# Kernel optimization log

Measured on AMD Instinct MI355X. Metric: run time of the kernel, lower is better.

The kernel has to match this reference:

```python
import jax, jax.numpy as jnp
import numpy as np

B, IN, HID, OUT, K = 4096, 1024, 2048, 256, 8
# pairwise (i, j), i != j, row-major order as in the torch loop
_PAIRS = np.array([(i, j) for i in range(K) for j in range(K) if i != j])  # [56, 2]
IDX_I = jnp.asarray(_PAIRS[:, 0])
IDX_J = jnp.asarray(_PAIRS[:, 1])


def setup_inputs() -> dict:
    key = jax.random.key(0)
    ks = jax.random.split(key, 13)
    s_in, s_hid, s_2o, s_o = IN ** -0.5, HID ** -0.5, (2 * OUT) ** -0.5, OUT ** -0.5
    return {
        "input": jax.random.normal(ks[0], (B, IN), jnp.float32),
        # 8 stacked branch MLPs
        "W1": jax.random.normal(ks[1], (K, IN, HID), jnp.float32) * s_in,
        "b1": jax.random.normal(ks[2], (K, HID), jnp.float32) * s_in,
        "W2": jax.random.normal(ks[3], (K, HID, OUT), jnp.float32) * s_hid,
        "b2": jax.random.normal(ks[4], (K, OUT), jnp.float32) * s_hid,
        # model_on: 2*OUT -> HID -> 1
        "Won1": jax.random.normal(ks[5], (2 * OUT, HID), jnp.float32) * s_2o,
        "bon1": jax.random.normal(ks[6], (HID,), jnp.float32) * s_2o,
        "Won2": jax.random.normal(ks[7], (HID, 1), jnp.float32) * s_hid,
        "bon2": jax.random.normal(ks[8], (1,), jnp.float32) * s_hid,
        # model_clear: OUT -> HID -> 1
        "Wc1": jax.random.normal(ks[9], (OUT, HID), jnp.float32) * s_o,
        "bc1": jax.random.normal(ks[10], (HID,), jnp.float32) * s_o,
        "Wc2": jax.random.normal(ks[11], (HID, 1), jnp.float32) * s_hid,
        "bc2": jax.random.normal(ks[12], (1,), jnp.float32) * s_hid,
    }


def reference(input, W1, b1, W2, b2, Won1, bon1, Won2, bon2, Wc1, bc1, Wc2, bc2):
    # 8 branch MLPs on the same input, as one grouped GEMM: [K, B, HID]
    h = jax.nn.relu(jnp.einsum('bi,kih->kbh', input, W1) + b1[:, None, :])
    emb = jnp.einsum('kbh,kho->kbo', h, W2) + b2[:, None, :]  # [K, B, OUT]

    # 56 pairwise concats -> model_on, batched: [56, B, 2*OUT]
    pair = jnp.concatenate([emb[IDX_I], emb[IDX_J]], axis=-1)
    ho = jax.nn.relu(jnp.einsum('pbf,fh->pbh', pair, Won1) + bon1)
    on = jnp.einsum('pbh,h->pb', ho, Won2[:, 0]) + bon2[0]  # [56, B]

    # 8 clear heads, batched: [8, B]
    hc = jax.nn.relu(jnp.einsum('kbo,oh->kbh', emb, Wc1) + bc1)
    clear = jnp.einsum('kbh,h->kb', hc, Wc2[:, 0]) + bc2[0]

    # torch concatenates [56 on-outputs, 8 clear-outputs] along dim=1 -> [B, 64]
    return jnp.concatenate([on, clear], axis=0).T
```

## Files before the change

kernel.cpp:

```cpp
#include <hip/hip_runtime.h>

typedef __attribute__((ext_vector_type(8))) short bf16x8;
typedef __attribute__((ext_vector_type(4))) float f32x4;
typedef __attribute__((ext_vector_type(8))) unsigned short u16x8;

__device__ __forceinline__ float bf2f(short s) {
  unsigned u = ((unsigned)(unsigned short)s) << 16;
  return __builtin_bit_cast(float, u);
}
__device__ __forceinline__ unsigned short f2bf(float f) {
  unsigned u = __builtin_bit_cast(unsigned, f);
  u = (u + 0x7fffu + ((u >> 16) & 1u)) >> 16;
  return (unsigned short)u;
}
__device__ __forceinline__ void gload16(const unsigned short* g, unsigned short* l) {
  __builtin_amdgcn_global_load_lds(
      (const __attribute__((address_space(1))) void*)g,
      (__attribute__((address_space(3))) void*)l, 16, 0, 0);
}

__global__ __launch_bounds__(256)
void prep_kernel(const float* __restrict__ input, const float* __restrict__ W1,
                 const float* __restrict__ W2, const float* __restrict__ Won1,
                 const float* __restrict__ Wc1,
                 unsigned short* __restrict__ inputb, unsigned short* __restrict__ W1T,
                 unsigned short* __restrict__ W2T, unsigned short* __restrict__ WcatT,
                 unsigned short* __restrict__ Wc1T) {
  int bid = blockIdx.x;
  const int t = threadIdx.x;
  if (bid < 2048) {
    long i = ((long)bid * 256 + t) * 8;
    float4 a = *(const float4*)(input + i);
    float4 b = *(const float4*)(input + i + 4);
    u16x8 o;
    o[0] = f2bf(a.x); o[1] = f2bf(a.y); o[2] = f2bf(a.z); o[3] = f2bf(a.w);
    o[4] = f2bf(b.x); o[5] = f2bf(b.y); o[6] = f2bf(b.z); o[7] = f2bf(b.w);
    *(u16x8*)(inputb + i) = o;
    return;
  }
  bid -= 2048;
  const float* src; unsigned short* dst;
  int R, C, tilesX, tilesY; long sb, db;
  if (bid < 16384) {
    src = W1; dst = W1T; R = 1024; C = 2048; tilesX = 64; tilesY = 32;
    sb = 2097152; db = 2097152;
  } else if ((bid -= 16384) < 4096) {
    src = W2; dst = W2T; R = 2048; C = 256; tilesX = 8; tilesY = 64;
    sb = 524288; db = 524288;
  } else if ((bid -= 4096) < 512) {
    src = Won1; dst = WcatT; R = 256; C = 2048; tilesX = 64; tilesY = 8;
    sb = 0; db = 0;
  } else if ((bid -= 512) < 512) {
    src = Won1 + 524288; dst = WcatT + (long)2048 * 256;
    R = 256; C = 2048; tilesX = 64; tilesY = 8; sb = 0; db = 0;
  } else {
    bid -= 512;
    src = Wc1; dst = Wc1T; R = 256; C = 2048; tilesX = 64; tilesY = 8;
    sb = 0; db = 0;
  }
  const int x = bid % tilesX;
  const int rem = bid / tilesX;
  const int y = rem % tilesY;
  const int z = rem / tilesY;
  src += (long)z * sb;
  dst += (long)z * db;
  __shared__ float tile[32][33];
  const int tx = t & 31, ty = t >> 5;
  const int bx = x * 32, by = y * 32;
  #pragma unroll
  for (int i = ty; i < 32; i += 8)
    tile[i][tx] = src[(long)(by + i) * C + bx + tx];
  __syncthreads();
  #pragma unroll
  for (int i = ty; i < 32; i += 8)
    dst[(long)(bx + i) * R + by + tx] = f2bf(tile[tx][i]);
}

template<bool HAS_BIAS, bool RELU>
__global__ __launch_bounds__(512, 1)
void gemm256(const unsigned short* __restrict__ A,
             const unsigned short* __restrict__ Bt,
             const float* __restrict__ bias,
             unsigned short* __restrict__ C,
             int N, int K, int nx, int ny, int GM,
             long sA, long sB, long sBias, long sC) {
  __shared__ unsigned short lds[65536];
  const int t = threadIdx.x;
  const int lane = t & 63;
  const int w = t >> 6, wr = w >> 2, wc = w & 3;

  const int nwg = gridDim.x;
  const int cpx = nwg >> 3;
  const int id = blockIdx.x;
  const int sw = (id & 7) * cpx + (id >> 3);
  const int z = sw / (nx * ny);
  const int rem = sw % (nx * ny);
  const int band = rem / (GM * nx);
  const int rr = rem % (GM * nx);
  const int y = band * GM + (rr % GM);
  const int x = rr / GM;
  const int m0 = y * 256, n0 = x * 256;

  A += (long)z * sA;
  Bt += (long)z * sB;
  C += (long)z * sC;

  const int NH = K >> 4;
  const int ITERS = K >> 7;

  const int sr0 = t >> 3;
  const int sc0 = (t & 7) * 16;
  const int cks0 = (((lane >> 4) * 16)) ^ ((lane & 7) << 4);
  const int cks1 = (64 + ((lane >> 4) * 16)) ^ ((lane & 7) << 4);
  const int aoff = wr * 16384 + (lane & 15) * 128;
  const int boff = 32768 + (wc >> 1) * 16384 + ((wc & 1) * 64 + (lane & 15)) * 128;

  f32x4 acc[8][4] = {};
  bf16x8 af[4][2];
  bf16x8 bfr[2][2][2];

#define STAGE(S) do { if ((S) < NH) {                                          \
    const int kt_ = (S) >> 2, slot_ = (S) & 3;                                 \
    const int base_ = ((kt_ & 1) << 16) + ((slot_ < 2) ? 32768 : 0)            \
                      + ((slot_ & 1) << 14);                                   \
    const unsigned short* gb_;                                                 \
    _Pragma("unroll")                                                          \
    for (int j_ = 0; j_ < 2; ++j_) {                                           \
      const int r_ = sr0 + j_ * 64;                                            \
      const int yc_ = sc0 ^ ((r_ & 7) << 4);                                   \
      if (slot_ < 2)                                                           \
        gb_ = Bt + (long)(n0 + (slot_ & 1) * 128 + r_) * K + kt_ * 64 + (yc_ >> 1); \
      else                                                                     \
        gb_ = A + (long)(m0 + (slot_ & 1) * 128 + r_) * K + kt_ * 64 + (yc_ >> 1);  \
      gload16(gb_, lds + (base_ >> 1) + j_ * 4096 + t * 8);                    \
    } } } while (0)

#define LDA_(BUF, HM) do { _Pragma("unroll")                                   \
    for (int mi_ = 0; mi_ < 4; ++mi_) {                                        \
      af[mi_][0] = *(const bf16x8*)((const char*)lds + (BUF) * 65536 + aoff + ((HM) * 4 + mi_) * 2048 + cks0); \
      af[mi_][1] = *(const bf16x8*)((const char*)lds + (BUF) * 65536 + aoff + ((HM) * 4 + mi_) * 2048 + cks1); \
    } } while (0)

#define LDB_(BUF, HN) do { _Pragma("unroll")                                   \
    for (int ni_ = 0; ni_ < 2; ++ni_) {                                        \
      bfr[HN][ni_][0] = *(const bf16x8*)((const char*)lds + (BUF) * 65536 + boff + ((HN) * 2 + ni_) * 2048 + cks0); \
      bfr[HN][ni_][1] = *(const bf16x8*)((const char*)lds + (BUF) * 65536 + boff + ((HN) * 2 + ni_) * 2048 + cks1); \
    } } while (0)

#define DO_MFMA(HM, HN) do { _Pragma("unroll")                                 \
    for (int mi_ = 0; mi_ < 4; ++mi_) { _Pragma("unroll")                      \
      for (int ni_ = 0; ni_ < 2; ++ni_) { _Pragma("unroll")                    \
        for (int ks_ = 0; ks_ < 2; ++ks_)                                      \
          acc[(HM) * 4 + mi_][(HN) * 2 + ni_] =                                \
            __builtin_amdgcn_mfma_f32_16x16x32_bf16(af[mi_][ks_], bfr[HN][ni_][ks_], \
                acc[(HM) * 4 + mi_][(HN) * 2 + ni_], 0, 0, 0);                 \
    } } } while (0)

#define PHASE(MB) do {                                                         \
    __builtin_amdgcn_s_barrier();                                              \
    asm volatile("s_waitcnt lgkmcnt(0)" ::: "memory");                         \
    __builtin_amdgcn_sched_barrier(0);                                         \
    __builtin_amdgcn_s_setprio(1);                                             \
    MB;                                                                        \
    __builtin_amdgcn_s_setprio(0);                                             \
    __builtin_amdgcn_s_barrier();                                              \
  } while (0)

  STAGE(0); STAGE(1); STAGE(2); STAGE(3);
  asm volatile("s_waitcnt vmcnt(4)" ::: "memory");
  STAGE(4); STAGE(5); STAGE(6);
  asm volatile("s_waitcnt vmcnt(6)" ::: "memory");
  __builtin_amdgcn_s_barrier();

  for (int i = 0; i < ITERS; ++i) {
    const int s0 = 7 + (i << 3);
    const bool last = (i == ITERS - 1);
    LDA_(0, 0); LDB_(0, 0); STAGE(s0 + 0);
    PHASE(DO_MFMA(0, 0));
    LDB_(0, 1);             STAGE(s0 + 1);
    PHASE(DO_MFMA(0, 1));
    LDA_(0, 1);             STAGE(s0 + 2);
    PHASE(DO_MFMA(1, 1));
                            STAGE(s0 + 3);
    if (last) asm volatile("s_waitcnt vmcnt(0)" ::: "memory");
    else      asm volatile("s_waitcnt vmcnt(6)" ::: "memory");
    PHASE(DO_MFMA(1, 0));
    LDA_(1, 0); LDB_(1, 0); STAGE(s0 + 4);
    PHASE(DO_MFMA(0, 0));
    LDB_(1, 1);             STAGE(s0 + 5);
    PHASE(DO_MFMA(0, 1));
    LDA_(1, 1);             STAGE(s0 + 6);
    PHASE(DO_MFMA(1, 1));
                            STAGE(s0 + 7);
    if (!last) asm volatile("s_waitcnt vmcnt(6)" ::: "memory");
    PHASE(DO_MFMA(1, 0));
  }

#undef STAGE
#undef LDA_
#undef LDB_
#undef DO_MFMA
#undef PHASE

  #pragma unroll
  for (int Mi = 0; Mi < 8; ++Mi) {
    #pragma unroll
    for (int Ni = 0; Ni < 4; ++Ni) {
      const int colg = n0 + wc * 64 + Ni * 16 + (lane & 15);
      float bv = 0.f;
      if (HAS_BIAS) bv = bias[(long)z * sBias + colg];
      #pragma unroll
      for (int r2 = 0; r2 < 4; ++r2) {
        const int rowg = m0 + wr * 128 + Mi * 16 + (lane >> 4) * 4 + r2;
        float v = acc[Mi][Ni][r2] + bv;
        if (RELU) v = fmaxf(v, 0.f);
        C[(long)rowg * N + colg] = f2bf(v);
      }
    }
  }
}

template<bool HAS_BIAS, bool RELU>
__global__ __launch_bounds__(256, 4)
void gemm_bm64(const unsigned short* __restrict__ A,
               const unsigned short* __restrict__ Bt,
               const float* __restrict__ bias,
               unsigned short* __restrict__ C,
               int N, int K, int nx, int ny, int GM,
               long sA, long sB, long sBias, long sC) {
  __shared__ unsigned short As[64 * 64];
  __shared__ unsigned short Bs[128 * 64];
  const int t = threadIdx.x;
  const int lane = t & 63;
  const int w = t >> 6, wr = w >> 1, wc = w & 1;

  const int nwg = gridDim.x;
  const int cpx = nwg >> 3;
  const int id = blockIdx.x;
  const int sw = (id & 7) * cpx + (id >> 3);
  const int z = sw / (nx * ny);
  const int rem = sw % (nx * ny);
  const int band = rem / (GM * nx);
  const int r = rem % (GM * nx);
  const int y = band * GM + (r % GM);
  const int x = r / GM;
  const int m0 = y * 64, n0 = x * 128;

  A += (long)z * sA;
  Bt += (long)z * sB;
  C += (long)z * sC;

  const int prow = lane >> 3;
  const int pcol = (lane & 7) * 8;

  f32x4 acc[2][4] = {};

  for (int kt = 0; kt < K; kt += 64) {
    __syncthreads();
    #pragma unroll
    for (int p = 0; p < 2; ++p) {
      const int rbase = p * 32 + w * 8;
      gload16(A + (long)(m0 + rbase + prow) * K + kt + pcol, As + rbase * 64);
    }
    #pragma unroll
    for (int p = 0; p < 4; ++p) {
      const int rbase = p * 32 + w * 8;
      gload16(Bt + (long)(n0 + rbase + prow) * K + kt + pcol, Bs + rbase * 64);
    }
    __syncthreads();
    #pragma unroll
    for (int ks = 0; ks < 2; ++ks) {
      bf16x8 af[2], bfr[4];
      #pragma unroll
      for (int mi = 0; mi < 2; ++mi) {
        const int row = wr * 32 + mi * 16 + (lane & 15);
        af[mi] = *(const bf16x8*)((const char*)As + row * 128 + ks * 64 + (lane >> 4) * 16);
      }
      #pragma unroll
      for (int ni = 0; ni < 4; ++ni) {
        const int row = wc * 64 + ni * 16 + (lane & 15);
        bfr[ni] = *(const bf16x8*)((const char*)Bs + row * 128 + ks * 64 + (lane >> 4) * 16);
      }
      #pragma unroll
      for (int mi = 0; mi < 2; ++mi)
        #pragma unroll
        for (int ni = 0; ni < 4; ++ni)
          acc[mi][ni] = __builtin_amdgcn_mfma_f32_16x16x32_bf16(af[mi], bfr[ni], acc[mi][ni], 0, 0, 0);
    }
  }

  #pragma unroll
  for (int mi = 0; mi < 2; ++mi) {
    #pragma unroll
    for (int ni = 0; ni < 4; ++ni) {
      const int colg = n0 + wc * 64 + ni * 16 + (lane & 15);
      float bv = 0.f;
      if (HAS_BIAS) bv = bias[(long)z * sBias + colg];
      #pragma unroll
      for (int r2 = 0; r2 < 4; ++r2) {
        const int rowg = m0 + wr * 32 + mi * 16 + (lane >> 4) * 4 + r2;
        float v = acc[mi][ni][r2] + bv;
        if (RELU) v = fmaxf(v, 0.f);
        C[(long)rowg * N + colg] = f2bf(v);
      }
    }
  }
}

__global__ __launch_bounds__(256, 3)
void clear_fused(const unsigned short* __restrict__ emb,
                 const unsigned short* __restrict__ Wc1T,
                 const float* __restrict__ bc1, const float* __restrict__ Wc2,
                 const float* __restrict__ bc2,
                 float* __restrict__ out, int M) {
  __shared__ unsigned short Ae[64 * 256];
  __shared__ unsigned short Bs[128 * 64];
  __shared__ float red[4][64];
  const int t = threadIdx.x;
  const int lane = t & 63;
  const int w = t >> 6;
  const int k = blockIdx.y;
  const int m0 = blockIdx.x * 64;
  const unsigned short* A = emb + ((long)k * M + m0) * 256;

  #pragma unroll
  for (int pass = 0; pass < 8; ++pass) {
    const int row = pass * 8 + (t >> 5);
    const int sc = t & 31;
    float4 v = *(const float4*)(A + (long)row * 256 + sc * 8);
    *(float4*)((char*)Ae + row * 512 + ((sc * 16) ^ ((row & 7) << 4))) = v;
  }

  float rsum[4][4] = {};

  for (int nt = 0; nt < 16; ++nt) {
    f32x4 acc[4][2] = {};
    for (int kt = 0; kt < 256; kt += 64) {
      __syncthreads();
      #pragma unroll
      for (int pass = 0; pass < 4; ++pass) {
        const int row = pass * 32 + (t >> 3);
        gload16(Wc1T + (long)(nt * 128 + row) * 256 + kt + (t & 7) * 8,
                Bs + row * 64 + (t & 7) * 8);
      }
      __syncthreads();
      #pragma unroll
      for (int ks = 0; ks < 2; ++ks) {
        bf16x8 af[4], bfr[2];
        #pragma unroll
        for (int mi = 0; mi < 4; ++mi) {
          const int row = mi * 16 + (lane & 15);
          const int ce = kt + ks * 32 + (lane >> 4) * 8;
          af[mi] = *(const bf16x8*)((const char*)Ae + row * 512 + ((ce * 2) ^ ((row & 7) << 4)));
        }
        #pragma unroll
        for (int ni = 0; ni < 2; ++ni) {
          const int row = w * 32 + ni * 16 + (lane & 15);
          bfr[ni] = *(const bf16x8*)((const char*)Bs + row * 128 + ks * 64 + (lane >> 4) * 16);
        }
        #pragma unroll
        for (int mi = 0; mi < 4; ++mi)
          #pragma unroll
          for (int ni = 0; ni < 2; ++ni)
            acc[mi][ni] = __builtin_amdgcn_mfma_f32_16x16x32_bf16(af[mi], bfr[ni], acc[mi][ni], 0, 0, 0);
      }
    }
    #pragma unroll
    for (int mi = 0; mi < 4; ++mi) {
      #pragma unroll
      for (int ni = 0; ni < 2; ++ni) {
        const int col = nt * 128 + w * 32 + ni * 16 + (lane & 15);
        const float bv = bc1[col], wv = Wc2[col];
        #pragma unroll
        for (int r = 0; r < 4; ++r)
          rsum[mi][r] += fmaxf(acc[mi][ni][r] + bv, 0.f) * wv;
      }
    }
  }

  #pragma unroll
  for (int off = 1; off < 16; off <<= 1)
    #pragma unroll
    for (int mi = 0; mi < 4; ++mi)
      #pragma unroll
      for (int r = 0; r < 4; ++r)
        rsum[mi][r] += __shfl_xor(rsum[mi][r], off, 64);
  if ((lane & 15) == 0) {
    #pragma unroll
    for (int mi = 0; mi < 4; ++mi)
      #pragma unroll
      for (int r = 0; r < 4; ++r)
        red[w][mi * 16 + (lane >> 4) * 4 + r] = rsum[mi][r];
  }
  __syncthreads();
  if (t < 64)
    out[(long)(m0 + t) * 64 + 56 + k] =
        red[0][t] + red[1][t] + red[2][t] + red[3][t] + bc2[0];
}

__global__ __launch_bounds__(256)
void pair_reduce_kernel(const unsigned short* __restrict__ UVT,
                        const float* __restrict__ bon1, const float* __restrict__ Won2,
                        const float* __restrict__ bon2,
                        float* __restrict__ out, int Mc) {
  __shared__ unsigned short uv[8 * 4096];
  const int b = blockIdx.x, t = threadIdx.x;
  const long kstride = (long)Mc * 4096;
  const unsigned short* src = UVT + (long)b * 4096;

  float4 ba = *(const float4*)(bon1 + t * 8);
  float4 bb = *(const float4*)(bon1 + t * 8 + 4);
  const float bsv[8] = {ba.x, ba.y, ba.z, ba.w, bb.x, bb.y, bb.z, bb.w};

  for (int k = 0; k < 8; ++k) {
    const unsigned short* s = src + (long)k * kstride;
    {
      const int c = t;
      const int byte = k * 8192 + ((c * 16) ^ ((k & 7) << 4));
      *(float4*)((char*)uv + byte) = *(const float4*)(s + c * 8);
    }
    {
      const int c = 256 + t;
      bf16x8 v = *(const bf16x8*)(s + c * 8);
      u16x8 o;
      #pragma unroll
      for (int e = 0; e < 8; ++e)
        o[e] = f2bf(bf2f(v[e]) + bsv[e]);
      const int byte = k * 8192 + ((c * 16) ^ ((k & 7) << 4));
      *(u16x8*)((char*)uv + byte) = o;
    }
  }
  __syncthreads();
  const int p = t & 63, q = t >> 6;
  float acc = 0.f;
  if (p < 56) {
    const int i = p / 7;
    const int jj = p % 7;
    const int j = jj + (jj >= i);
    const char* ubase = (const char*)uv + i * 8192;
    const char* vbase = (const char*)uv + j * 8192;
    const int uswz = (i & 7) << 4, vswz = (j & 7) << 4;
    for (int it = 0; it < 64; ++it) {
      const int h = q * 512 + it * 8;
      bf16x8 uu = *(const bf16x8*)(ubase + ((h * 2) ^ uswz));
      bf16x8 vv = *(const bf16x8*)(vbase + ((4096 + h * 2) ^ vswz));
      float4 wa = *(const float4*)(Won2 + h);
      float4 wb = *(const float4*)(Won2 + h + 4);
      float wv[8] = {wa.x, wa.y, wa.z, wa.w, wb.x, wb.y, wb.z, wb.w};
      #pragma unroll
      for (int e = 0; e < 8; ++e) {
        float xv = bf2f(uu[e]) + bf2f(vv[e]);
        acc += fmaxf(xv, 0.f) * wv[e];
      }
    }
  }
  __syncthreads();
  float* red = (float*)uv;
  red[q * 64 + p] = acc;
  __syncthreads();
  if (t < 56)
    out[(long)b * 64 + t] = red[t] + red[64 + t] + red[128 + t] + red[192 + t] + bon2[0];
}

extern "C" void kernel_launch(void* const* d_in, const int* in_sizes, int n_in,
                              void* d_out, int out_size, void* d_ws, size_t ws_size,
                              hipStream_t stream) {
  (void)in_sizes; (void)n_in; (void)out_size;
  const float* input = (const float*)d_in[0];
  const float* W1    = (const float*)d_in[1];
  const float* b1    = (const float*)d_in[2];
  const float* W2    = (const float*)d_in[3];
  const float* b2    = (const float*)d_in[4];
  const float* Won1  = (const float*)d_in[5];
  const float* bon1  = (const float*)d_in[6];
  const float* Won2  = (const float*)d_in[7];
  const float* bon2  = (const float*)d_in[8];
  const float* Wc1   = (const float*)d_in[9];
  const float* bc1   = (const float*)d_in[10];
  const float* Wc2   = (const float*)d_in[11];
  const float* bc2   = (const float*)d_in[12];
  float* out = (float*)d_out;

  char* base = (char*)d_ws;
  unsigned short* inputb = (unsigned short*)(base);
  unsigned short* W1T    = (unsigned short*)(base + 8388608L);
  unsigned short* W2T    = (unsigned short*)(base + 41943040L);
  unsigned short* WcatT  = (unsigned short*)(base + 50331648L);
  unsigned short* Wc1T   = (unsigned short*)(base + 52428800L);
  unsigned short* hbuf   = (unsigned short*)(base + 53477376L);
  unsigned short* embbuf = (unsigned short*)(base + 187695104L);
  unsigned short* UVTbuf = (unsigned short*)(base + 204472320L);

  int Mc = 512;
  const int mopts[3] = {4096, 2048, 1024};
  for (int oi = 0; oi < 3; ++oi) {
    if (204472320L + (long)mopts[oi] * 65536L <= (long)ws_size) { Mc = mopts[oi]; break; }
  }
  const int nc = 4096 / Mc;

  prep_kernel<<<dim3(24064), 256, 0, stream>>>(input, W1, W2, Won1, Wc1,
                                               inputb, W1T, W2T, WcatT, Wc1T);

  gemm256<true, true><<<dim3(8 * 16 * 8), 512, 0, stream>>>(
      inputb, W1T, b1, hbuf, 2048, 1024, 8, 16, 4,
      0L, (long)2048 * 1024, 2048L, (long)4096 * 2048);

  gemm_bm64<true, false><<<dim3(2 * 64 * 8), 256, 0, stream>>>(
      hbuf, W2T, b2, embbuf, 256, 2048, 2, 64, 4,
      (long)4096 * 2048, (long)256 * 2048, 256L, (long)4096 * 256);

  clear_fused<<<dim3(64, 8), 256, 0, stream>>>(embbuf, Wc1T, bc1, Wc2, bc2, out, 4096);

  for (int cc = 0; cc < nc; ++cc) {
    const long b0 = (long)cc * Mc;
    const int nyc = Mc / 256;
    const int GM3 = (nyc % 4 == 0) ? 4 : ((nyc % 2 == 0) ? 2 : 1);
    gemm256<false, false><<<dim3(16 * nyc * 8), 512, 0, stream>>>(
        embbuf + b0 * 256, WcatT, nullptr, UVTbuf, 4096, 256, 16, nyc, GM3,
        (long)4096 * 256, 0L, 0L, (long)Mc * 4096);
    pair_reduce_kernel<<<dim3(Mc), 256, 0, stream>>>(
        UVTbuf, bon1, Won2, bon2, out + b0 * 64, Mc);
  }
}
```

Measured before the change: 601.5 us.

## Replace bm64 second GEMM with pipelined 128x256 tile kernel and interleave UVT layout

Replaces the simple 64x128-tile GEMM for the branch second layer with a 512-thread 128x256-tile kernel. The new kernel uses swizzled LDS, double buffering and phased MFMA scheduling like the main gemm256. It also adds an ldc parameter so the pair GEMM writes UVT interleaved per batch row across the 8 branches. That makes pair_reduce read each row's 8 slices contiguously. Partial lgkmcnt waits are inserted so the MFMA phases can overlap LDS reads, at the cost of more complex sync that is riskier to get correct.

```diff
diff --git a/kernel.cpp b/kernel.cpp
--- a/kernel.cpp
+++ b/kernel.cpp
@@ -82,7 +82,7 @@
              const unsigned short* __restrict__ Bt,
              const float* __restrict__ bias,
              unsigned short* __restrict__ C,
-             int N, int K, int nx, int ny, int GM,
+             int N, int K, int ldc, int nx, int ny, int GM,
              long sA, long sB, long sBias, long sC) {
   __shared__ unsigned short lds[65536];
   const int t = threadIdx.x;
@@ -176,6 +176,7 @@
     const int s0 = 7 + (i << 3);
     const bool last = (i == ITERS - 1);
     LDA_(0, 0); LDB_(0, 0); STAGE(s0 + 0);
+    asm volatile("s_waitcnt lgkmcnt(8)" ::: "memory");
     PHASE(DO_MFMA(0, 0));
     LDB_(0, 1);             STAGE(s0 + 1);
     PHASE(DO_MFMA(0, 1));
@@ -186,6 +187,7 @@
     else      asm volatile("s_waitcnt vmcnt(6)" ::: "memory");
     PHASE(DO_MFMA(1, 0));
     LDA_(1, 0); LDB_(1, 0); STAGE(s0 + 4);
+    asm volatile("s_waitcnt lgkmcnt(8)" ::: "memory");
     PHASE(DO_MFMA(0, 0));
     LDB_(1, 1);             STAGE(s0 + 5);
     PHASE(DO_MFMA(0, 1));
@@ -214,25 +216,24 @@
         const int rowg = m0 + wr * 128 + Mi * 16 + (lane >> 4) * 4 + r2;
         float v = acc[Mi][Ni][r2] + bv;
         if (RELU) v = fmaxf(v, 0.f);
-        C[(long)rowg * N + colg] = f2bf(v);
+        C[(long)rowg * ldc + colg] = f2bf(v);
       }
     }
   }
 }
 
 template<bool HAS_BIAS, bool RELU>
-__global__ __launch_bounds__(256, 4)
-void gemm_bm64(const unsigned short* __restrict__ A,
-               const unsigned short* __restrict__ Bt,
-               const float* __restrict__ bias,
-               unsigned short* __restrict__ C,
-               int N, int K, int nx, int ny, int GM,
-               long sA, long sB, long sBias, long sC) {
-  __shared__ unsigned short As[64 * 64];
-  __shared__ unsigned short Bs[128 * 64];
+__global__ __launch_bounds__(512, 1)
+void gemm_bm128(const unsigned short* __restrict__ A,
+                const unsigned short* __restrict__ Bt,
+                const float* __restrict__ bias,
+                unsigned short* __restrict__ C,
+                int N, int K, int nx, int ny, int GM,
+                long sA, long sB, long sBias, long sC) {
+  __shared__ unsigned short lds[49152];
   const int t = threadIdx.x;
   const int lane = t & 63;
-  const int w = t >> 6, wr = w >> 1, wc = w & 1;
+  const int w = t >> 6, wr = w >> 2, wc = w & 3;
 
   const int nwg = gridDim.x;
   const int cpx = nwg >> 3;
@@ -241,56 +242,115 @@
   const int z = sw / (nx * ny);
   const int rem = sw % (nx * ny);
   const int band = rem / (GM * nx);
-  const int r = rem % (GM * nx);
-  const int y = band * GM + (r % GM);
-  const int x = r / GM;
-  const int m0 = y * 64, n0 = x * 128;
+  const int rr = rem % (GM * nx);
+  const int y = band * GM + (rr % GM);
+  const int x = rr / GM;
+  const int m0 = y * 128, n0 = x * 256;
 
   A += (long)z * sA;
   Bt += (long)z * sB;
   C += (long)z * sC;
 
-  const int prow = lane >> 3;
-  const int pcol = (lane & 7) * 8;
-
-  f32x4 acc[2][4] = {};
-
-  for (int kt = 0; kt < K; kt += 64) {
-    __syncthreads();
-    #pragma unroll
-    for (int p = 0; p < 2; ++p) {
-      const int rbase = p * 32 + w * 8;
-      gload16(A + (long)(m0 + rbase + prow) * K + kt + pcol, As + rbase * 64);
-    }
-    #pragma unroll
-    for (int p = 0; p < 4; ++p) {
-      const int rbase = p * 32 + w * 8;
-      gload16(Bt + (long)(n0 + rbase + prow) * K + kt + pcol, Bs + rbase * 64);
-    }
-    __syncthreads();
-    #pragma unroll
-    for (int ks = 0; ks < 2; ++ks) {
-      bf16x8 af[2], bfr[4];
-      #pragma unroll
-      for (int mi = 0; mi < 2; ++mi) {
-        const int row = wr * 32 + mi * 16 + (lane & 15);
-        af[mi] = *(const bf16x8*)((const char*)As + row * 128 + ks * 64 + (lane >> 4) * 16);
-      }
-      #pragma unroll
-      for (int ni = 0; ni < 4; ++ni) {
-        const int row = wc * 64 + ni * 16 + (lane & 15);
-        bfr[ni] = *(const bf16x8*)((const char*)Bs + row * 128 + ks * 64 + (lane >> 4) * 16);
-      }
-      #pragma unroll
-      for (int mi = 0; mi < 2; ++mi)
-        #pragma unroll
-        for (int ni = 0; ni < 4; ++ni)
-          acc[mi][ni] = __builtin_amdgcn_mfma_f32_16x16x32_bf16(af[mi], bfr[ni], acc[mi][ni], 0, 0, 0);
-    }
-  }
+  const int NH = K >> 4;
+  const int ITERS = K >> 7;
+
+  const int sr0 = t >> 3;
+  const int sc0 = (t & 7) * 16;
+  const int cks0 = (((lane >> 4) * 16)) ^ ((lane & 7) << 4);
+  const int cks1 = (64 + ((lane >> 4) * 16)) ^ ((lane & 7) << 4);
+  const int abase = 32768 + wr * 8192 + (lane & 15) * 128;
+  const int bbase = (wc >> 1) * 16384 + ((wc & 1) * 64 + (lane & 15)) * 128;
+
+  f32x4 acc[4][4] = {};
+  bf16x8 af[4][2];
+  bf16x8 bfr[2][2];
+
+#define STAGE(S) do { if ((S) < NH) {                                          \
+    const int kt_ = (S) >> 2, slot_ = (S) & 3;                                 \
+    const int bufb_ = (kt_ & 1) * 49152;                                       \
+    if (slot_ < 2) {                                                           \
+      _Pragma("unroll")                                                        \
+      for (int j_ = 0; j_ < 2; ++j_) {                                         \
+        const int r_ = sr0 + j_ * 64;                                          \
+        const int yc_ = sc0 ^ ((r_ & 7) << 4);                                 \
+        gload16(Bt + (long)(n0 + slot_ * 128 + r_) * K + kt_ * 64 + (yc_ >> 1),\
+                lds + ((bufb_ + slot_ * 16384 + j_ * 8192) >> 1) + t * 8);     \
+      }                                                                        \
+    } else {                                                                   \
+      const int yc_ = sc0 ^ ((sr0 & 7) << 4);                                  \
+      gload16(A + (long)(m0 + (slot_ & 1) * 64 + sr0) * K + kt_ * 64 + (yc_ >> 1), \
+              lds + ((bufb_ + 32768 + (slot_ & 1) * 8192) >> 1) + t * 8);      \
+    } } } while (0)
+
+#define LDA_(BUF) do { _Pragma("unroll")                                       \
+    for (int mi_ = 0; mi_ < 4; ++mi_) {                                        \
+      af[mi_][0] = *(const bf16x8*)((const char*)lds + (BUF) * 49152 + abase + mi_ * 2048 + cks0); \
+      af[mi_][1] = *(const bf16x8*)((const char*)lds + (BUF) * 49152 + abase + mi_ * 2048 + cks1); \
+    } } while (0)
+
+#define LDB_(BUF, HN) do { _Pragma("unroll")                                   \
+    for (int ni_ = 0; ni_ < 2; ++ni_) {                                        \
+      bfr[ni_][0] = *(const bf16x8*)((const char*)lds + (BUF) * 49152 + bbase + ((HN) * 2 + ni_) * 2048 + cks0); \
+      bfr[ni_][1] = *(const bf16x8*)((const char*)lds + (BUF) * 49152 + bbase + ((HN) * 2 + ni_) * 2048 + cks1); \
+    } } while (0)
+
+#define DO_MFMA(HN) do { _Pragma("unroll")                                     \
+    for (int mi_ = 0; mi_ < 4; ++mi_) { _Pragma("unroll")                      \
+      for (int ni_ = 0; ni_ < 2; ++ni_) { _Pragma("unroll")                    \
+        for (int ks_ = 0; ks_ < 2; ++ks_)                                      \
+          acc[mi_][(HN) * 2 + ni_] =                                           \
+            __builtin_amdgcn_mfma_f32_16x16x32_bf16(af[mi_][ks_], bfr[ni_][ks_], \
+                acc[mi_][(HN) * 2 + ni_], 0, 0, 0);                            \
+    } } } while (0)
+
+#define PHASE(MB) do {                                                         \
+    __builtin_amdgcn_s_barrier();                                              \
+    asm volatile("s_waitcnt lgkmcnt(0)" ::: "memory");                         \
+    __builtin_amdgcn_sched_barrier(0);                                         \
+    __builtin_amdgcn_s_setprio(1);                                             \
+    MB;                                                                        \
+    __builtin_amdgcn_s_setprio(0);                                             \
+    __builtin_amdgcn_s_barrier();                                              \
+  } while (0)
+
+  STAGE(0); STAGE(2); STAGE(3); STAGE(1);
+  STAGE(4); STAGE(6); STAGE(7);
+  asm volatile("s_waitcnt vmcnt(6)" ::: "memory");
+  __builtin_amdgcn_s_barrier();
+
+  for (int i = 0; i < ITERS; ++i) {
+    const int s0 = i << 3;
+    const bool last = (i == ITERS - 1);
+    LDA_(0); LDB_(0, 0);
+    STAGE(s0 + 5);
+    asm volatile("s_waitcnt lgkmcnt(8)" ::: "memory");
+    asm volatile("s_waitcnt vmcnt(6)" ::: "memory");
+    PHASE(DO_MFMA(0));
+    LDB_(0, 1);
+    STAGE(s0 + 8); STAGE(s0 + 10); STAGE(s0 + 11);
+    if (last) asm volatile("s_waitcnt vmcnt(0)" ::: "memory");
+    else      asm volatile("s_waitcnt vmcnt(6)" ::: "memory");
+    PHASE(DO_MFMA(1));
+    LDA_(1); LDB_(1, 0);
+    STAGE(s0 + 9);
+    asm volatile("s_waitcnt lgkmcnt(8)" ::: "memory");
+    if (last) asm volatile("s_waitcnt vmcnt(0)" ::: "memory");
+    else      asm volatile("s_waitcnt vmcnt(6)" ::: "memory");
+    PHASE(DO_MFMA(0));
+    LDB_(1, 1);
+    STAGE(s0 + 12); STAGE(s0 + 14); STAGE(s0 + 15);
+    if (!last) asm volatile("s_waitcnt vmcnt(6)" ::: "memory");
+    PHASE(DO_MFMA(1));
+  }
+
+#undef STAGE
+#undef LDA_
+#undef LDB_
+#undef DO_MFMA
+#undef PHASE
 
   #pragma unroll
-  for (int mi = 0; mi < 2; ++mi) {
+  for (int mi = 0; mi < 4; ++mi) {
     #pragma unroll
     for (int ni = 0; ni < 4; ++ni) {
       const int colg = n0 + wc * 64 + ni * 16 + (lane & 15);
@@ -298,7 +358,7 @@
       if (HAS_BIAS) bv = bias[(long)z * sBias + colg];
       #pragma unroll
       for (int r2 = 0; r2 < 4; ++r2) {
-        const int rowg = m0 + wr * 32 + mi * 16 + (lane >> 4) * 4 + r2;
+        const int rowg = m0 + wr * 64 + mi * 16 + (lane >> 4) * 4 + r2;
         float v = acc[mi][ni][r2] + bv;
         if (RELU) v = fmaxf(v, 0.f);
         C[(long)rowg * N + colg] = f2bf(v);
@@ -405,15 +465,14 @@
                         float* __restrict__ out, int Mc) {
   __shared__ unsigned short uv[8 * 4096];
   const int b = blockIdx.x, t = threadIdx.x;
-  const long kstride = (long)Mc * 4096;
-  const unsigned short* src = UVT + (long)b * 4096;
+  const unsigned short* src = UVT + (long)b * 32768;
 
   float4 ba = *(const float4*)(bon1 + t * 8);
   float4 bb = *(const float4*)(bon1 + t * 8 + 4);
   const float bsv[8] = {ba.x, ba.y, ba.z, ba.w, bb.x, bb.y, bb.z, bb.w};
 
   for (int k = 0; k < 8; ++k) {
-    const unsigned short* s = src + (long)k * kstride;
+    const unsigned short* s = src + (long)k * 4096;
     {
       const int c = t;
       const int byte = k * 8192 + ((c * 16) ^ ((k & 7) << 4));
@@ -502,11 +561,11 @@
                                                inputb, W1T, W2T, WcatT, Wc1T);
 
   gemm256<true, true><<<dim3(8 * 16 * 8), 512, 0, stream>>>(
-      inputb, W1T, b1, hbuf, 2048, 1024, 8, 16, 4,
+      inputb, W1T, b1, hbuf, 2048, 1024, 2048, 8, 16, 4,
       0L, (long)2048 * 1024, 2048L, (long)4096 * 2048);
 
-  gemm_bm64<true, false><<<dim3(2 * 64 * 8), 256, 0, stream>>>(
-      hbuf, W2T, b2, embbuf, 256, 2048, 2, 64, 4,
+  gemm_bm128<true, false><<<dim3(256), 512, 0, stream>>>(
+      hbuf, W2T, b2, embbuf, 256, 2048, 1, 32, 4,
       (long)4096 * 2048, (long)256 * 2048, 256L, (long)4096 * 256);
 
   clear_fused<<<dim3(64, 8), 256, 0, stream>>>(embbuf, Wc1T, bc1, Wc2, bc2, out, 4096);
@@ -516,8 +575,8 @@
     const int nyc = Mc / 256;
     const int GM3 = (nyc % 4 == 0) ? 4 : ((nyc % 2 == 0) ? 2 : 1);
     gemm256<false, false><<<dim3(16 * nyc * 8), 512, 0, stream>>>(
-        embbuf + b0 * 256, WcatT, nullptr, UVTbuf, 4096, 256, 16, nyc, GM3,
-        (long)4096 * 256, 0L, 0L, (long)Mc * 4096);
+        embbuf + b0 * 256, WcatT, nullptr, UVTbuf, 4096, 256, 32768, 16, nyc, GM3,
+        (long)4096 * 256, 0L, 0L, 4096L);
     pair_reduce_kernel<<<dim3(Mc), 256, 0, stream>>>(
         UVTbuf, bon1, Won2, bon2, out + b0 * 64, Mc);
   }
```

New measurement: 583.0 us. 1.03x faster.
